# Kernel optimization log

Measured on AMD Instinct MI355X. Metric: run time of the kernel, lower is better.

## Reference

```python
import jax, jax.numpy as jnp
import numpy as np

N_NODES = 50000
N_EDGES = 800000
IN_FEAT = 256
OUT_FEAT = 256
NUM_RELS = 64
NUM_BASES = 8


def setup_inputs() -> dict:
    key = jax.random.key(0)
    ks = jax.random.split(key, 9)
    x = jax.random.normal(ks[0], (N_NODES, IN_FEAT), dtype=jnp.float32)
    src = jax.random.randint(ks[1], (N_EDGES,), 0, N_NODES, dtype=jnp.int32)
    dst = jax.random.randint(ks[2], (N_EDGES,), 0, N_NODES, dtype=jnp.int32)
    etypes = jax.random.randint(ks[3], (N_EDGES,), 0, NUM_RELS, dtype=jnp.int32)
    norm = jax.random.uniform(ks[4], (N_EDGES, 1), dtype=jnp.float32)
    # glorot-style params
    s_w = (6.0 / (IN_FEAT + OUT_FEAT)) ** 0.5
    weight = jax.random.uniform(ks[5], (NUM_BASES, IN_FEAT, OUT_FEAT), jnp.float32, -s_w, s_w)
    s_c = (6.0 / (NUM_RELS + NUM_BASES)) ** 0.5
    w_comp = jax.random.uniform(ks[6], (NUM_RELS, NUM_BASES), jnp.float32, -s_c, s_c)
    h_bias = jnp.zeros((OUT_FEAT,), jnp.float32)
    loop_weight = jax.random.uniform(ks[7], (IN_FEAT, OUT_FEAT), jnp.float32, -s_w, s_w)
    return {"x": x, "src": src, "dst": dst, "etypes": etypes, "norm": norm,
            "weight": weight, "w_comp": w_comp, "h_bias": h_bias,
            "loop_weight": loop_weight}


def reference(x, src, dst, etypes, norm, weight, w_comp, h_bias, loop_weight):
    # Basis regularizer with num_bases < num_rels:
    #   W_r = sum_b w_comp[r, b] * V_b
    # Per-edge message: msg_e = (x[src_e] @ W_{etype_e}) * norm_e,
    # aggregated by sum onto destination nodes. Since the map is linear,
    # we aggregate per basis first, then apply V_b (8 dense GEMMs).
    n_nodes = x.shape[0]
    coef = w_comp[etypes]                      # [E, B] per-edge basis coeffs
    xs = x[src] * norm                         # [E, D] normalized source feats
    out = jnp.zeros((n_nodes, weight.shape[2]), x.dtype)
    for b in range(weight.shape[0]):           # small fixed loop over bases
        agg = jax.ops.segment_sum(xs * coef[:, b:b + 1], dst,
                                  num_segments=n_nodes)   # [N, D]
        out = out + agg @ weight[b]            # [N, O]
    out = out + h_bias + x @ loop_weight       # bias + self-loop
    return jax.nn.relu(out)
```

## Files before the change

### kernel.cpp

```cpp
#include <hip/hip_runtime.h>
#include <hip/hip_bf16.h>
#include <stdint.h>

#define N_NODES 50000
#define N_EDGES 800000
#define IN_FEAT 256
#define OUT_FEAT 256
#define NUM_RELS 64
#define NUM_BASES 8
#define KTOT 2304
#define MP 50176
#define SCAN_BLKS 196
#define ROWB 4624

typedef __attribute__((ext_vector_type(8))) __bf16 bf16x8;
typedef __attribute__((ext_vector_type(4))) __bf16 bf16x4;
typedef __attribute__((ext_vector_type(4))) float f32x4;
typedef __attribute__((ext_vector_type(2))) float f32x2;

__global__ void k_prex(const float* __restrict__ x, __bf16* __restrict__ xb) {
  int i = blockIdx.x * 256 + threadIdx.x;
  const float4* xp = (const float4*)x;
  float4 u = xp[i * 2], v = xp[i * 2 + 1];
  bf16x8 o;
  o[0] = (__bf16)u.x; o[1] = (__bf16)u.y; o[2] = (__bf16)u.z; o[3] = (__bf16)u.w;
  o[4] = (__bf16)v.x; o[5] = (__bf16)v.y; o[6] = (__bf16)v.z; o[7] = (__bf16)v.w;
  *(bf16x8*)(xb + (size_t)i * 8) = o;
}

__global__ void k_count(const int* __restrict__ dst, int* __restrict__ deg) {
  int e = blockIdx.x * 256 + threadIdx.x;
  atomicAdd(&deg[dst[e]], 1);
}

__global__ void k_scan1(const int* __restrict__ deg, int* __restrict__ offs,
                        int* __restrict__ bsum) {
  __shared__ int s[256];
  int t = threadIdx.x;
  int i = blockIdx.x * 256 + t;
  int v = (i < N_NODES) ? deg[i] : 0;
  s[t] = v;
  __syncthreads();
  for (int d = 1; d < 256; d <<= 1) {
    int y = (t >= d) ? s[t - d] : 0;
    __syncthreads();
    s[t] += y;
    __syncthreads();
  }
  if (i < N_NODES) offs[i] = s[t] - v;
  if (t == 255) bsum[blockIdx.x] = s[255];
}

__global__ void k_scan3(int* __restrict__ offs, const int* __restrict__ bsum,
                        int* __restrict__ fill) {
  __shared__ int s[256];
  int t = threadIdx.x;
  s[t] = (t < SCAN_BLKS && t < blockIdx.x) ? bsum[t] : 0;
  __syncthreads();
  for (int d = 128; d; d >>= 1) {
    if (t < d) s[t] += s[t + d];
    __syncthreads();
  }
  int base = s[0];
  int i = blockIdx.x * 256 + t;
  if (i < N_NODES) {
    int o = offs[i] + base;
    offs[i] = o;
    fill[i] = o;
  }
}

__global__ void k_scatter(const int* __restrict__ dst, const int* __restrict__ srcv,
                          const int* __restrict__ ety, const float* __restrict__ norm,
                          int* __restrict__ fill, uint2* __restrict__ erec) {
  int e = blockIdx.x * 256 + threadIdx.x;
  int pos = atomicAdd(&fill[dst[e]], 1);
  erec[pos] = make_uint2((unsigned)srcv[e] | ((unsigned)ety[e] << 16),
                         __float_as_uint(norm[e]));
}

__global__ void k_prepwf(const float* __restrict__ weight, const float* __restrict__ loop_w,
                         __bf16* __restrict__ Wf) {
  int tid = blockIdx.x * 256 + threadIdx.x;
  int lane6 = tid & 63;
  int F = tid >> 6;
  int kt2 = F >> 4;
  int nf = F & 15;
  int o = nf * 16 + (lane6 & 15);
  int rbase = kt2 * 32 + (lane6 >> 4) * 8;
  bf16x8 v;
#pragma unroll
  for (int j = 0; j < 8; ++j) {
    int r = rbase + j;
    float f = (r < 2048) ? weight[(size_t)r * 256 + o]
                         : loop_w[(size_t)(r - 2048) * 256 + o];
    v[j] = (__bf16)f;
  }
  *(bf16x8*)(Wf + (size_t)tid * 8) = v;
}

#define AGGE(R, XV, ACC)                                                      \
  do {                                                                        \
    int et_ = __builtin_amdgcn_readfirstlane((int)((R).x >> 16));             \
    float nm_ = __uint_as_float((R).y);                                       \
    f32x2 v0_ = {__uint_as_float((XV).x << 16) * nm_,                         \
                 __uint_as_float((XV).x & 0xffff0000u) * nm_};                 \
    f32x2 v1_ = {__uint_as_float((XV).y << 16) * nm_,                         \
                 __uint_as_float((XV).y & 0xffff0000u) * nm_};                 \
    f32x4 cl_ = *(const f32x4*)(w_comp + et_ * 8);                            \
    f32x4 ch_ = *(const f32x4*)(w_comp + et_ * 8 + 4);                        \
    _Pragma("unroll") for (int b = 0; b < 4; ++b) {                           \
      ACC[b][0] += v0_ * cl_[b];                                              \
      ACC[b][1] += v1_ * cl_[b];                                              \
      ACC[b + 4][0] += v0_ * ch_[b];                                          \
      ACC[b + 4][1] += v1_ * ch_[b];                                          \
    }                                                                         \
  } while (0)

#define EDGE4(RP, I, ACC)                                                     \
  do {                                                                        \
    uint2 r0_ = (RP)[(I) + 0], r1_ = (RP)[(I) + 1];                           \
    uint2 r2_ = (RP)[(I) + 2], r3_ = (RP)[(I) + 3];                           \
    uint2 x0_ = *(const uint2*)(xb + (size_t)(r0_.x & 0xffffu) * IN_FEAT + lo4);\
    uint2 x1_ = *(const uint2*)(xb + (size_t)(r1_.x & 0xffffu) * IN_FEAT + lo4);\
    uint2 x2_ = *(const uint2*)(xb + (size_t)(r2_.x & 0xffffu) * IN_FEAT + lo4);\
    uint2 x3_ = *(const uint2*)(xb + (size_t)(r3_.x & 0xffffu) * IN_FEAT + lo4);\
    AGGE(r0_, x0_, ACC); AGGE(r1_, x1_, ACC);                                 \
    AGGE(r2_, x2_, ACC); AGGE(r3_, x3_, ACC);                                 \
  } while (0)

#define EDGE1(RP, I, ACC)                                                     \
  do {                                                                        \
    uint2 r_ = (RP)[(I)];                                                     \
    uint2 x_ = *(const uint2*)(xb + (size_t)(r_.x & 0xffffu) * IN_FEAT + lo4);\
    AGGE(r_, x_, ACC);                                                        \
  } while (0)

#define WRITE_ROW(ACC, R, NODE)                                               \
  do {                                                                        \
    char* rowp_ = sA + (size_t)(R) * ROWB;                                    \
    _Pragma("unroll") for (int b = 0; b < 8; ++b) {                           \
      int cp_ = b * 32 + (lane >> 1);                                         \
      bf16x4 o_;                                                              \
      o_[0] = (__bf16)ACC[b][0][0]; o_[1] = (__bf16)ACC[b][0][1];             \
      o_[2] = (__bf16)ACC[b][1][0]; o_[3] = (__bf16)ACC[b][1][1];             \
      *(bf16x4*)(rowp_ + cp_ * 16 + (lane & 1) * 8) = o_;                     \
    }                                                                         \
    uint2 xv_ = ((NODE) < N_NODES)                                            \
        ? *(const uint2*)(xb + (size_t)(NODE) * IN_FEAT + lo4)                \
        : make_uint2(0u, 0u);                                                 \
    int cx_ = 256 + (lane >> 1);                                              \
    *(uint2*)(rowp_ + cx_ * 16 + (lane & 1) * 8) = xv_;                       \
  } while (0)

#define AGG_PAIR(NA, NB, RA, RB)                                              \
  do {                                                                        \
    f32x2 acca[8][2], accb[8][2];                                             \
    _Pragma("unroll") for (int b = 0; b < 8; ++b) {                           \
      acca[b][0] = f32x2{0.f, 0.f}; acca[b][1] = f32x2{0.f, 0.f};             \
      accb[b][0] = f32x2{0.f, 0.f}; accb[b][1] = f32x2{0.f, 0.f};             \
    }                                                                         \
    int i0a = 0, ca = 0, i0b = 0, cb = 0;                                     \
    if ((NA) < N_NODES) {                                                     \
      i0a = __builtin_amdgcn_readfirstlane(offs[NA]);                         \
      ca  = __builtin_amdgcn_readfirstlane(fin[NA]) - i0a;                    \
    }                                                                         \
    if ((NB) < N_NODES) {                                                     \
      i0b = __builtin_amdgcn_readfirstlane(offs[NB]);                         \
      cb  = __builtin_amdgcn_readfirstlane(fin[NB]) - i0b;                    \
    }                                                                         \
    const uint2* rpa = erec + i0a;                                            \
    const uint2* rpb = erec + i0b;                                            \
    int ia = 0, ib = 0;                                                       \
    int mm = (ca < cb ? ca : cb) & ~3;                                        \
    for (; ia < mm; ia += 4, ib += 4) {                                       \
      EDGE4(rpa, ia, acca);                                                   \
      EDGE4(rpb, ib, accb);                                                   \
    }                                                                         \
    for (; ia + 4 <= ca; ia += 4) EDGE4(rpa, ia, acca);                       \
    for (; ib + 4 <= cb; ib += 4) EDGE4(rpb, ib, accb);                       \
    for (; ia < ca; ++ia) EDGE1(rpa, ia, acca);                               \
    for (; ib < cb; ++ib) EDGE1(rpb, ib, accb);                               \
    WRITE_ROW(acca, RA, NA);                                                  \
    WRITE_ROW(accb, RB, NB);                                                  \
  } while (0)

__global__ __launch_bounds__(1024, 4) void k_fused(
    const __bf16* __restrict__ xb, const float* __restrict__ w_comp,
    const int* __restrict__ offs, const int* __restrict__ fin,
    const uint2* __restrict__ erec, const __bf16* __restrict__ Wf,
    const float* __restrict__ bias, float* __restrict__ out) {
  __shared__ __align__(16) char sA[32 * ROWB];

  int t = threadIdx.x;
  int wid = t >> 6, lane = t & 63;
  int tm = blockIdx.x;
  int lo4 = lane * 4;

  {
    int na = tm * 32 + wid * 2;
    AGG_PAIR(na, na + 1, wid * 2, wid * 2 + 1);
  }
  __syncthreads();

  int frow = lane & 15, g = lane >> 4;
  const char* ap0 = (const char*)sA + (size_t)frow * ROWB + g * 16;
  const char* ap1 = (const char*)sA + (size_t)(16 + frow) * ROWB + g * 16;

  f32x4 acc2[2];
  acc2[0] = f32x4{0.f, 0.f, 0.f, 0.f};
  acc2[1] = f32x4{0.f, 0.f, 0.f, 0.f};

  bf16x8 Aa[2], Ab[2], B0, B1;

#define LD_A(KT, D)                                                           \
  do {                                                                        \
    D[0] = *(const bf16x8*)(ap0 + (KT) * 64);                                 \
    D[1] = *(const bf16x8*)(ap1 + (KT) * 64);                                 \
  } while (0)

#define LD_B(KT, D)                                                           \
  do {                                                                        \
    D = *(const bf16x8*)(Wf + (size_t)((KT) * 16 + wid) * 512 + lane * 8);    \
  } while (0)

#define FMA2(AS, BS)                                                          \
  do {                                                                        \
    acc2[0] = __builtin_amdgcn_mfma_f32_16x16x32_bf16(AS[0], BS, acc2[0], 0, 0, 0); \
    acc2[1] = __builtin_amdgcn_mfma_f32_16x16x32_bf16(AS[1], BS, acc2[1], 0, 0, 0); \
  } while (0)

  LD_A(0, Aa); LD_B(0, B0);
  for (int kt = 0; kt < 72; kt += 2) {
    int n1 = kt + 1;
    int n2 = (kt + 2 < 72) ? kt + 2 : 71;
    LD_A(n1, Ab); LD_B(n1, B1); FMA2(Aa, B0);
    LD_A(n2, Aa); LD_B(n2, B0); FMA2(Ab, B1);
  }
#undef LD_A
#undef LD_B
#undef FMA2

  int r0 = (lane >> 4) * 4;
  int c0 = lane & 15;
  int col = wid * 16 + c0;
  float bv = bias[col];
#pragma unroll
  for (int mf = 0; mf < 2; ++mf) {
    int rowb = tm * 32 + mf * 16 + r0;
#pragma unroll
    for (int j = 0; j < 4; ++j) {
      int row = rowb + j;
      if (row < N_NODES) {
        float v = acc2[mf][j] + bv;
        out[(size_t)row * OUT_FEAT + col] = v > 0.f ? v : 0.f;
      }
    }
  }
}

extern "C" void kernel_launch(void* const* d_in, const int* in_sizes, int n_in,
                              void* d_out, int out_size, void* d_ws, size_t ws_size,
                              hipStream_t stream) {
  const float* x      = (const float*)d_in[0];
  const int*   src    = (const int*)d_in[1];
  const int*   dst    = (const int*)d_in[2];
  const int*   ety    = (const int*)d_in[3];
  const float* norm   = (const float*)d_in[4];
  const float* weight = (const float*)d_in[5];
  const float* w_comp = (const float*)d_in[6];
  const float* h_bias = (const float*)d_in[7];
  const float* loop_w = (const float*)d_in[8];
  float* out = (float*)d_out;

  char* ws = (char*)d_ws;
  __bf16* xb = (__bf16*)ws;
  size_t off = (size_t)MP * IN_FEAT * 2;
  __bf16* Wf = (__bf16*)(ws + off);
  off += (size_t)256 * KTOT * 2;
  uint2* erec = (uint2*)(ws + off);
  off += (size_t)N_EDGES * 8;
  int* deg   = (int*)(ws + off);
  int* offs  = deg + N_NODES;
  int* fill  = offs + N_NODES;
  int* bsum  = fill + N_NODES;

  hipMemsetAsync(deg, 0, N_NODES * sizeof(int), stream);
  k_prex<<<(N_NODES * IN_FEAT / 8) / 256, 256, 0, stream>>>(x, xb);
  k_count<<<N_EDGES / 256, 256, 0, stream>>>(dst, deg);
  k_scan1<<<SCAN_BLKS, 256, 0, stream>>>(deg, offs, bsum);
  k_scan3<<<SCAN_BLKS, 256, 0, stream>>>(offs, bsum, fill);
  k_scatter<<<N_EDGES / 256, 256, 0, stream>>>(dst, src, ety, norm, fill, erec);
  k_prepwf<<<288, 256, 0, stream>>>(weight, loop_w, Wf);
  k_fused<<<MP / 32, 1024, 0, stream>>>(xb, w_comp, offs, fill, erec, Wf, h_bias, out);
}
```

Baseline: 297.8 us.

## Merge prep kernels into one launch and XOR-swizzle the shared A tile

The x-to-bf16 conversion, degree counting and weight repacking now run in a single kernel, which removes two kernel launches. The shared-memory A tile moves from a padded row-major layout to K-slab-major 4 KB planes with an XOR swizzle on 16-byte chunks, meant to avoid LDS bank conflicts on both the aggregation writes and the MFMA operand reads. The prep kernel's grid covers 1.6M threads, so the edge and weight work rely on index guards, and the swizzle indexing must match between writer and reader.

Measured after the change: 281.0 us. 1.06x faster.

```diff
diff --git a/kernel.cpp b/kernel.cpp
--- a/kernel.cpp
+++ b/kernel.cpp
@@ -11,14 +11,16 @@
 #define KTOT 2304
 #define MP 50176
 #define SCAN_BLKS 196
-#define ROWB 4624
 
 typedef __attribute__((ext_vector_type(8))) __bf16 bf16x8;
 typedef __attribute__((ext_vector_type(4))) __bf16 bf16x4;
 typedef __attribute__((ext_vector_type(4))) float f32x4;
 typedef __attribute__((ext_vector_type(2))) float f32x2;
 
-__global__ void k_prex(const float* __restrict__ x, __bf16* __restrict__ xb) {
+__global__ void k_prep(const float* __restrict__ x, __bf16* __restrict__ xb,
+                       const int* __restrict__ dst, int* __restrict__ deg,
+                       const float* __restrict__ weight, const float* __restrict__ loop_w,
+                       __bf16* __restrict__ Wf) {
   int i = blockIdx.x * 256 + threadIdx.x;
   const float4* xp = (const float4*)x;
   float4 u = xp[i * 2], v = xp[i * 2 + 1];
@@ -26,11 +28,24 @@
   o[0] = (__bf16)u.x; o[1] = (__bf16)u.y; o[2] = (__bf16)u.z; o[3] = (__bf16)u.w;
   o[4] = (__bf16)v.x; o[5] = (__bf16)v.y; o[6] = (__bf16)v.z; o[7] = (__bf16)v.w;
   *(bf16x8*)(xb + (size_t)i * 8) = o;
-}
-
-__global__ void k_count(const int* __restrict__ dst, int* __restrict__ deg) {
-  int e = blockIdx.x * 256 + threadIdx.x;
-  atomicAdd(&deg[dst[e]], 1);
+  if (i < N_EDGES) atomicAdd(&deg[dst[i]], 1);
+  if (i < 73728) {
+    int lane6 = i & 63;
+    int F = i >> 6;
+    int kt2 = F >> 4;
+    int nf = F & 15;
+    int oc = nf * 16 + (lane6 & 15);
+    int rbase = kt2 * 32 + (lane6 >> 4) * 8;
+    bf16x8 w;
+#pragma unroll
+    for (int j = 0; j < 8; ++j) {
+      int r = rbase + j;
+      float f = (r < 2048) ? weight[(size_t)r * 256 + oc]
+                           : loop_w[(size_t)(r - 2048) * 256 + oc];
+      w[j] = (__bf16)f;
+    }
+    *(bf16x8*)(Wf + (size_t)i * 8) = w;
+  }
 }
 
 __global__ void k_scan1(const int* __restrict__ deg, int* __restrict__ offs,
@@ -79,26 +94,6 @@
                          __float_as_uint(norm[e]));
 }
 
-__global__ void k_prepwf(const float* __restrict__ weight, const float* __restrict__ loop_w,
-                         __bf16* __restrict__ Wf) {
-  int tid = blockIdx.x * 256 + threadIdx.x;
-  int lane6 = tid & 63;
-  int F = tid >> 6;
-  int kt2 = F >> 4;
-  int nf = F & 15;
-  int o = nf * 16 + (lane6 & 15);
-  int rbase = kt2 * 32 + (lane6 >> 4) * 8;
-  bf16x8 v;
-#pragma unroll
-  for (int j = 0; j < 8; ++j) {
-    int r = rbase + j;
-    float f = (r < 2048) ? weight[(size_t)r * 256 + o]
-                         : loop_w[(size_t)(r - 2048) * 256 + o];
-    v[j] = (__bf16)f;
-  }
-  *(bf16x8*)(Wf + (size_t)tid * 8) = v;
-}
-
 #define AGGE(R, XV, ACC)                                                      \
   do {                                                                        \
     int et_ = __builtin_amdgcn_readfirstlane((int)((R).x >> 16));             \
@@ -138,19 +133,19 @@
 
 #define WRITE_ROW(ACC, R, NODE)                                               \
   do {                                                                        \
-    char* rowp_ = sA + (size_t)(R) * ROWB;                                    \
+    char* base_ = sA + (size_t)(R) * 128 +                                    \
+                  ((((lane >> 1) & 7) ^ ((R) & 7)) * 16 + (lane & 1) * 8);    \
+    int ktl_ = lane >> 4;                                                     \
     _Pragma("unroll") for (int b = 0; b < 8; ++b) {                           \
-      int cp_ = b * 32 + (lane >> 1);                                         \
       bf16x4 o_;                                                              \
       o_[0] = (__bf16)ACC[b][0][0]; o_[1] = (__bf16)ACC[b][0][1];             \
       o_[2] = (__bf16)ACC[b][1][0]; o_[3] = (__bf16)ACC[b][1][1];             \
-      *(bf16x4*)(rowp_ + cp_ * 16 + (lane & 1) * 8) = o_;                     \
+      *(bf16x4*)(base_ + (b * 4 + ktl_) * 4096) = o_;                         \
     }                                                                         \
     uint2 xv_ = ((NODE) < N_NODES)                                            \
         ? *(const uint2*)(xb + (size_t)(NODE) * IN_FEAT + lo4)                \
         : make_uint2(0u, 0u);                                                 \
-    int cx_ = 256 + (lane >> 1);                                              \
-    *(uint2*)(rowp_ + cx_ * 16 + (lane & 1) * 8) = xv_;                       \
+    *(uint2*)(base_ + (32 + ktl_) * 4096) = xv_;                              \
   } while (0)
 
 #define AGG_PAIR(NA, NB, RA, RB)                                              \
@@ -190,7 +185,7 @@
     const int* __restrict__ offs, const int* __restrict__ fin,
     const uint2* __restrict__ erec, const __bf16* __restrict__ Wf,
     const float* __restrict__ bias, float* __restrict__ out) {
-  __shared__ __align__(16) char sA[32 * ROWB];
+  __shared__ __align__(16) char sA[36 * 4096];
 
   int t = threadIdx.x;
   int wid = t >> 6, lane = t & 63;
@@ -204,8 +199,10 @@
   __syncthreads();
 
   int frow = lane & 15, g = lane >> 4;
-  const char* ap0 = (const char*)sA + (size_t)frow * ROWB + g * 16;
-  const char* ap1 = (const char*)sA + (size_t)(16 + frow) * ROWB + g * 16;
+  int kb0 = ((g ^ (frow & 7)) << 4);
+  int kb1 = (((4 + g) ^ (frow & 7)) << 4);
+  const char* ap0 = (const char*)sA + frow * 128;
+  const char* ap1 = (const char*)sA + (16 + frow) * 128;
 
   f32x4 acc2[2];
   acc2[0] = f32x4{0.f, 0.f, 0.f, 0.f};
@@ -213,15 +210,16 @@
 
   bf16x8 Aa[2], Ab[2], B0, B1;
 
-#define LD_A(KT, D)                                                           \
-  do {                                                                        \
-    D[0] = *(const bf16x8*)(ap0 + (KT) * 64);                                 \
-    D[1] = *(const bf16x8*)(ap1 + (KT) * 64);                                 \
-  } while (0)
-
-#define LD_B(KT, D)                                                           \
-  do {                                                                        \
-    D = *(const bf16x8*)(Wf + (size_t)((KT) * 16 + wid) * 512 + lane * 8);    \
+#define LD_A(K2, HALF, D)                                                     \
+  do {                                                                        \
+    int off_ = ((K2) >> 1) * 4096 + ((HALF) ? kb1 : kb0);                     \
+    D[0] = *(const bf16x8*)(ap0 + off_);                                      \
+    D[1] = *(const bf16x8*)(ap1 + off_);                                      \
+  } while (0)
+
+#define LD_B(K2, D)                                                           \
+  do {                                                                        \
+    D = *(const bf16x8*)(Wf + (size_t)((K2) * 16 + wid) * 512 + lane * 8);    \
   } while (0)
 
 #define FMA2(AS, BS)                                                          \
@@ -230,12 +228,12 @@
     acc2[1] = __builtin_amdgcn_mfma_f32_16x16x32_bf16(AS[1], BS, acc2[1], 0, 0, 0); \
   } while (0)
 
-  LD_A(0, Aa); LD_B(0, B0);
+  LD_A(0, 0, Aa); LD_B(0, B0);
   for (int kt = 0; kt < 72; kt += 2) {
     int n1 = kt + 1;
-    int n2 = (kt + 2 < 72) ? kt + 2 : 71;
-    LD_A(n1, Ab); LD_B(n1, B1); FMA2(Aa, B0);
-    LD_A(n2, Aa); LD_B(n2, B0); FMA2(Ab, B1);
+    int n2 = (kt + 2 < 72) ? kt + 2 : 70;
+    LD_A(n1, 1, Ab); LD_B(n1, B1); FMA2(Aa, B0);
+    LD_A(n2, 0, Aa); LD_B(n2, B0); FMA2(Ab, B1);
   }
 #undef LD_A
 #undef LD_B
@@ -286,11 +284,10 @@
   int* bsum  = fill + N_NODES;
 
   hipMemsetAsync(deg, 0, N_NODES * sizeof(int), stream);
-  k_prex<<<(N_NODES * IN_FEAT / 8) / 256, 256, 0, stream>>>(x, xb);
-  k_count<<<N_EDGES / 256, 256, 0, stream>>>(dst, deg);
+  k_prep<<<(N_NODES * IN_FEAT / 8) / 256, 256, 0, stream>>>(x, xb, dst, deg,
+                                                            weight, loop_w, Wf);
   k_scan1<<<SCAN_BLKS, 256, 0, stream>>>(deg, offs, bsum);
   k_scan3<<<SCAN_BLKS, 256, 0, stream>>>(offs, bsum, fill);
   k_scatter<<<N_EDGES / 256, 256, 0, stream>>>(dst, src, ety, norm, fill, erec);
-  k_prepwf<<<288, 256, 0, stream>>>(weight, loop_w, Wf);
   k_fused<<<MP / 32, 1024, 0, stream>>>(xb, w_comp, offs, fill, erec, Wf, h_bias, out);
 }
```
